# Performance work log

Measured on AMD Instinct MI355X. Metric: run time of the kernel, lower is better.

## Reference

```python
import jax, jax.numpy as jnp
import numpy as np

B = 8192          # batch
LATENT = 32       # latent_dim
H = 64            # hidden_size
SEQ_LEN = 180
NUM_CLASSES = 6
IN = 2            # GRU input size (zeros) / output features


def setup_inputs() -> dict:
    key = jax.random.key(0)
    ks = jax.random.split(key, 12)
    s_fc = 1.0 / np.sqrt(LATENT + H)
    s_rnn = 1.0 / np.sqrt(H)
    return {
        "z": jax.random.normal(ks[0], (B, LATENT), dtype=jnp.float32),
        "labels": jax.random.randint(ks[1], (B,), 0, NUM_CLASSES),
        "embed_w": jax.random.normal(ks[2], (NUM_CLASSES, H), dtype=jnp.float32),
        "fc_w": jax.random.uniform(ks[3], (H, LATENT + H), jnp.float32, -s_fc, s_fc),
        "fc_b": jax.random.uniform(ks[4], (H,), jnp.float32, -s_fc, s_fc),
        "w_ih": jax.random.uniform(ks[5], (3 * H, IN), jnp.float32, -s_rnn, s_rnn),
        "w_hh": jax.random.uniform(ks[6], (3 * H, H), jnp.float32, -s_rnn, s_rnn),
        "b_ih": jax.random.uniform(ks[7], (3 * H,), jnp.float32, -s_rnn, s_rnn),
        "b_hh": jax.random.uniform(ks[8], (3 * H,), jnp.float32, -s_rnn, s_rnn),
        "out_w": jax.random.uniform(ks[9], (IN, H), jnp.float32, -s_rnn, s_rnn),
        "out_b": jax.random.uniform(ks[10], (IN,), jnp.float32, -s_rnn, s_rnn),
    }


def reference(z, labels, embed_w, fc_w, fc_b, w_ih, w_hh, b_ih, b_hh, out_w, out_b):
    # h0 = tanh(fc([z, embed(labels)]))  -> [B, H]
    cond = embed_w[labels]
    h0 = jnp.tanh(jnp.concatenate([z, cond], axis=1) @ fc_w.T + fc_b)

    # GRU input is all zeros, so the input-side gates are constant per step:
    # gi = x_t @ w_ih.T + b_ih = b_ih  (kept faithful to torch GRU math)
    i_r, i_z, i_n = jnp.split(b_ih, 3)

    def step(h, _):
        gh = h @ w_hh.T + b_hh                      # [B, 3H]
        h_r, h_z, h_n = jnp.split(gh, 3, axis=-1)
        r = jax.nn.sigmoid(i_r + h_r)
        zg = jax.nn.sigmoid(i_z + h_z)
        n = jnp.tanh(i_n + r * h_n)
        h_new = (1.0 - zg) * n + zg * h
        return h_new, h_new

    _, hs = jax.lax.scan(step, h0, None, length=SEQ_LEN)  # [S, B, H]
    # out linear: [B, S, 2]
    return jnp.einsum("sbh,oh->bso", hs, out_w) + out_b
```

## Files before the change

kernel.cpp:

```cpp
#include <hip/hip_runtime.h>

#define NBATCH 8192
#define HDIM   64
#define SEQ    180
#define MT     16
#define NC     2
#define SB     72
#define XSP    100

typedef __bf16 bf16x8 __attribute__((ext_vector_type(8)));
typedef __bf16 bf16x4 __attribute__((ext_vector_type(4)));
typedef float  f32x4  __attribute__((ext_vector_type(4)));

#define L2E 1.44269504088896340736f

__device__ __forceinline__ float tanh_f(float x) {
    float e = __builtin_amdgcn_exp2f((2.0f * L2E) * x);
    return 1.0f - 2.0f * __builtin_amdgcn_rcpf(1.0f + e);
}

#define MFMA __builtin_amdgcn_mfma_f32_16x16x32_bf16

__device__ __forceinline__ f32x4 gru_epi(f32x4 aR, f32x4 aZ, f32x4 aN,
        f32x4 cR4, f32x4 cZ4, f32x4 bn4, f32x4 cN4, f32x4 one4,
        f32x4 hprev, __bf16* Nh, int wboff) {
    f32x4 tR = aR * (-L2E) + cR4;
    f32x4 tZ = aZ * (-L2E) + cZ4;
    f32x4 eR, eZ;
#pragma unroll
    for (int r = 0; r < 4; ++r) {
        eR[r] = __builtin_amdgcn_exp2f(tR[r]);
        eZ[r] = __builtin_amdgcn_exp2f(tZ[r]);
    }
    eR = eR + one4;
    eZ = eZ + one4;
    f32x4 rg, zg;
#pragma unroll
    for (int r = 0; r < 4; ++r) {
        rg[r] = __builtin_amdgcn_rcpf(eR[r]);
        zg[r] = __builtin_amdgcn_rcpf(eZ[r]);
    }
    f32x4 mm = aN + bn4;
    f32x4 tN = (rg * mm) * (2.0f * L2E) + cN4;
    f32x4 eN;
#pragma unroll
    for (int r = 0; r < 4; ++r) eN[r] = __builtin_amdgcn_exp2f(tN[r]);
    eN = eN + one4;
    f32x4 dd;
#pragma unroll
    for (int r = 0; r < 4; ++r) dd[r] = __builtin_amdgcn_rcpf(eN[r]);
    f32x4 ng = dd * (-2.0f) + one4;
    f32x4 hn = zg * (hprev - ng) + ng;
    bf16x4 hp;
#pragma unroll
    for (int r = 0; r < 4; ++r) hp[r] = (__bf16)hn[r];
    *(bf16x4*)(Nh + wboff) = hp;
    return hn;
}

__global__ __launch_bounds__(256) void gru_all(
        const float* __restrict__ z, const int* __restrict__ labels,
        const float* __restrict__ embed_w, const float* __restrict__ fc_w,
        const float* __restrict__ fc_b, const float* __restrict__ w_hh,
        const float* __restrict__ b_ih, const float* __restrict__ b_hh,
        const float* __restrict__ out_w, const float* __restrict__ out_b,
        float* __restrict__ out) {
    __shared__ __align__(16) __bf16 hbuf[NC][2][MT * SB];
    __shared__ __align__(16) float  xs[NC * MT * XSP];

    const int t = threadIdx.x;
    const int w = t >> 6;
    const int l = t & 63;
    const int q = l >> 4;
    const int n16 = l & 15;
    const int jg = 16 * w + n16;
    const int jb = 16 * w + 4 * q;
    const int bbase = blockIdx.x * (NC * MT);

    for (int c = t; c < NC * MT * 24; c += 256) {
        int m = c / 24, kk = (c % 24) * 4;
        f32x4 v;
        if (kk < 32) v = *(const f32x4*)(z + (size_t)(bbase + m) * 32 + kk);
        else         v = *(const f32x4*)(embed_w + labels[bbase + m] * 64 + (kk - 32));
        *(f32x4*)(xs + m * XSP + kk) = v;
    }

    bf16x8 whi[3][2];
#pragma unroll
    for (int g = 0; g < 3; ++g) {
        const float* pr = w_hh + (g * 64 + jg) * HDIM;
#pragma unroll
        for (int ks = 0; ks < 2; ++ks) {
            const float* p = pr + ks * 32 + q * 8;
            f32x4 va = *(const f32x4*)(p);
            f32x4 vb = *(const f32x4*)(p + 4);
#pragma unroll
            for (int j2 = 0; j2 < 4; ++j2) {
                whi[g][ks][j2]     = (__bf16)va[j2];
                whi[g][ks][4 + j2] = (__bf16)vb[j2];
            }
        }
    }

    bf16x8 obhi[2];
#pragma unroll
    for (int ks = 0; ks < 2; ++ks) {
        f32x4 va = {0.f, 0.f, 0.f, 0.f}, vb = {0.f, 0.f, 0.f, 0.f};
        if (n16 < 2) {
            va = *(const f32x4*)(out_w + n16 * 64 + ks * 32 + q * 8);
            vb = *(const f32x4*)(out_w + n16 * 64 + ks * 32 + q * 8 + 4);
        }
#pragma unroll
        for (int j2 = 0; j2 < 4; ++j2) {
            obhi[ks][j2]     = (__bf16)va[j2];
            obhi[ks][4 + j2] = (__bf16)vb[j2];
        }
    }
    const f32x4 obias = (q == 0) ? f32x4{out_b[0], out_b[1], 0.f, 0.f}
                                 : f32x4{0.f, 0.f, 0.f, 0.f};
    const f32x4 kZ = {0.f, 0.f, 0.f, 0.f};
    const f32x4 one4 = {1.f, 1.f, 1.f, 1.f};

    const bool ostorer = (q == 0) && ((n16 >> 2) == w);

    const f32x4 bihR = *(const f32x4*)(b_ih + jb);
    const f32x4 bhhR = *(const f32x4*)(b_hh + jb);
    const f32x4 bihZ = *(const f32x4*)(b_ih + 64 + jb);
    const f32x4 bhhZ = *(const f32x4*)(b_hh + 64 + jb);
    const f32x4 cR4 = (bihR + bhhR) * (-L2E);
    const f32x4 cZ4 = (bihZ + bhhZ) * (-L2E);
    const f32x4 bn4 = *(const f32x4*)(b_hh + 128 + jb);
    const f32x4 cN4 = (*(const f32x4*)(b_ih + 128 + jb)) * (2.0f * L2E);

    const int rdoff = n16 * SB + q * 8;
    const int wboff = n16 * SB + jb;
    float* opbA = out + (size_t)(bbase + n16) * (SEQ * 2);
    float* opbB = out + (size_t)(bbase + MT + n16) * (SEQ * 2);

    __syncthreads();

    f32x4 hpA, hpB;
    {
        f32x4 aA = *(const f32x4*)(fc_b + jb);
        f32x4 aB = aA;
        for (int kc = 0; kc < 24; ++kc) {
            f32x4 xvA = *(const f32x4*)(xs + n16 * XSP + kc * 4);
            f32x4 xvB = *(const f32x4*)(xs + (MT + n16) * XSP + kc * 4);
#pragma unroll
            for (int r = 0; r < 4; ++r) {
                f32x4 wv = *(const f32x4*)(fc_w + (size_t)(jb + r) * 96 + kc * 4);
                aA[r] += wv[0] * xvA[0] + wv[1] * xvA[1] + wv[2] * xvA[2] + wv[3] * xvA[3];
                aB[r] += wv[0] * xvB[0] + wv[1] * xvB[1] + wv[2] * xvB[2] + wv[3] * xvB[3];
            }
        }
        bf16x4 ha, hb;
#pragma unroll
        for (int r = 0; r < 4; ++r) {
            hpA[r] = tanh_f(aA[r]); ha[r] = (__bf16)hpA[r];
            hpB[r] = tanh_f(aB[r]); hb[r] = (__bf16)hpB[r];
        }
        *(bf16x4*)(hbuf[0][0] + wboff) = ha;
        *(bf16x4*)(hbuf[1][0] + wboff) = hb;
    }
    __syncthreads();

    for (int u = 0; u < SEQ / 2; ++u) {
#pragma unroll
        for (int s = 0; s < 2; ++s) {
            const __bf16* HA = hbuf[0][s];
            __bf16*       NA = hbuf[0][s ^ 1];
            const __bf16* HB = hbuf[1][s];
            __bf16*      NhB = hbuf[1][s ^ 1];

            bf16x8 a0 = *(const bf16x8*)(HA + rdoff);
            bf16x8 a1 = *(const bf16x8*)(HA + rdoff + 32);
            bf16x8 c0 = *(const bf16x8*)(HB + rdoff);
            bf16x8 c1 = *(const bf16x8*)(HB + rdoff + 32);

            f32x4 ArA = MFMA(whi[0][0], a0, kZ, 0, 0, 0);
            f32x4 AzA = MFMA(whi[1][0], a0, kZ, 0, 0, 0);
            f32x4 AnA = MFMA(whi[2][0], a0, kZ, 0, 0, 0);
            f32x4 ArB = MFMA(whi[0][0], c0, kZ, 0, 0, 0);
            f32x4 AzB = MFMA(whi[1][0], c0, kZ, 0, 0, 0);
            f32x4 AnB = MFMA(whi[2][0], c0, kZ, 0, 0, 0);
            ArA = MFMA(whi[0][1], a1, ArA, 0, 0, 0);
            AzA = MFMA(whi[1][1], a1, AzA, 0, 0, 0);
            AnA = MFMA(whi[2][1], a1, AnA, 0, 0, 0);
            ArB = MFMA(whi[0][1], c1, ArB, 0, 0, 0);
            AzB = MFMA(whi[1][1], c1, AzB, 0, 0, 0);
            AnB = MFMA(whi[2][1], c1, AnB, 0, 0, 0);

            {
                f32x4 oA = obias;
                oA = MFMA(obhi[0], a0, oA, 0, 0, 0);
                oA = MFMA(obhi[1], a1, oA, 0, 0, 0);
                f32x4 oB = obias;
                oB = MFMA(obhi[0], c0, oB, 0, 0, 0);
                oB = MFMA(obhi[1], c1, oB, 0, 0, 0);
                if ((u | s) != 0 && ostorer) {
                    *(float2*)(opbA + (4 * u + 2 * s - 2)) = make_float2(oA[0], oA[1]);
                    *(float2*)(opbB + (4 * u + 2 * s - 2)) = make_float2(oB[0], oB[1]);
                }
            }

            hpA = gru_epi(ArA, AzA, AnA, cR4, cZ4, bn4, cN4, one4, hpA, NA,  wboff);
            hpB = gru_epi(ArB, AzB, AnB, cR4, cZ4, bn4, cN4, one4, hpB, NhB, wboff);

            __syncthreads();
        }
    }

    {
        bf16x8 a0 = *(const bf16x8*)(hbuf[0][0] + rdoff);
        bf16x8 a1 = *(const bf16x8*)(hbuf[0][0] + rdoff + 32);
        bf16x8 c0 = *(const bf16x8*)(hbuf[1][0] + rdoff);
        bf16x8 c1 = *(const bf16x8*)(hbuf[1][0] + rdoff + 32);
        f32x4 oA = obias;
        oA = MFMA(obhi[0], a0, oA, 0, 0, 0);
        oA = MFMA(obhi[1], a1, oA, 0, 0, 0);
        f32x4 oB = obias;
        oB = MFMA(obhi[0], c0, oB, 0, 0, 0);
        oB = MFMA(obhi[1], c1, oB, 0, 0, 0);
        if (ostorer) {
            *(float2*)(opbA + (SEQ - 1) * 2) = make_float2(oA[0], oA[1]);
            *(float2*)(opbB + (SEQ - 1) * 2) = make_float2(oB[0], oB[1]);
        }
    }
}

extern "C" void kernel_launch(void* const* d_in, const int* in_sizes, int n_in,
                              void* d_out, int out_size, void* d_ws, size_t ws_size,
                              hipStream_t stream) {
    (void)in_sizes; (void)n_in; (void)out_size; (void)d_ws; (void)ws_size;
    const float* z       = (const float*)d_in[0];
    const int*   labels  = (const int*)d_in[1];
    const float* embed_w = (const float*)d_in[2];
    const float* fc_w    = (const float*)d_in[3];
    const float* fc_b    = (const float*)d_in[4];
    const float* w_hh    = (const float*)d_in[6];
    const float* b_ih    = (const float*)d_in[7];
    const float* b_hh    = (const float*)d_in[8];
    const float* out_w   = (const float*)d_in[9];
    const float* out_b   = (const float*)d_in[10];
    float* out = (float*)d_out;

    gru_all<<<NBATCH / (NC * MT), 256, 0, stream>>>(z, labels, embed_w, fc_w, fc_b,
                                                    w_hh, b_ih, b_hh, out_w, out_b, out);
}
```

Before: 189.9 us.

## Defer output projection a step, merge GRU epilogue divisions, use LDS-only barrier

The output projection for the previous step's hidden state is now computed with registers kept from the prior iteration, issued before the current gate MFMAs. This takes it off the critical path between the LDS read and the gate math. The GRU update is rewritten so the z-gate sigmoid and the tanh combine into a single reciprocal, cutting the transcendental count. The batch A/B epilogues are interleaved and the inner loop is unrolled by 4. __syncthreads is replaced by an inline s_waitcnt lgkmcnt(0)+s_barrier, which risks subtle ordering issues and adds register pressure from the saved operands.

```diff
diff --git a/kernel.cpp b/kernel.cpp
--- a/kernel.cpp
+++ b/kernel.cpp
@@ -1,6 +1,6 @@
 #include <hip/hip_runtime.h>
 
-#define NBATCH 8192
+#define NB     8192
 #define HDIM   64
 #define SEQ    180
 #define MT     16
@@ -21,42 +21,7 @@
 
 #define MFMA __builtin_amdgcn_mfma_f32_16x16x32_bf16
 
-__device__ __forceinline__ f32x4 gru_epi(f32x4 aR, f32x4 aZ, f32x4 aN,
-        f32x4 cR4, f32x4 cZ4, f32x4 bn4, f32x4 cN4, f32x4 one4,
-        f32x4 hprev, __bf16* Nh, int wboff) {
-    f32x4 tR = aR * (-L2E) + cR4;
-    f32x4 tZ = aZ * (-L2E) + cZ4;
-    f32x4 eR, eZ;
-#pragma unroll
-    for (int r = 0; r < 4; ++r) {
-        eR[r] = __builtin_amdgcn_exp2f(tR[r]);
-        eZ[r] = __builtin_amdgcn_exp2f(tZ[r]);
-    }
-    eR = eR + one4;
-    eZ = eZ + one4;
-    f32x4 rg, zg;
-#pragma unroll
-    for (int r = 0; r < 4; ++r) {
-        rg[r] = __builtin_amdgcn_rcpf(eR[r]);
-        zg[r] = __builtin_amdgcn_rcpf(eZ[r]);
-    }
-    f32x4 mm = aN + bn4;
-    f32x4 tN = (rg * mm) * (2.0f * L2E) + cN4;
-    f32x4 eN;
-#pragma unroll
-    for (int r = 0; r < 4; ++r) eN[r] = __builtin_amdgcn_exp2f(tN[r]);
-    eN = eN + one4;
-    f32x4 dd;
-#pragma unroll
-    for (int r = 0; r < 4; ++r) dd[r] = __builtin_amdgcn_rcpf(eN[r]);
-    f32x4 ng = dd * (-2.0f) + one4;
-    f32x4 hn = zg * (hprev - ng) + ng;
-    bf16x4 hp;
-#pragma unroll
-    for (int r = 0; r < 4; ++r) hp[r] = (__bf16)hn[r];
-    *(bf16x4*)(Nh + wboff) = hp;
-    return hn;
-}
+#define BAR_LDS() asm volatile("s_waitcnt lgkmcnt(0)\n\ts_barrier" ::: "memory")
 
 __global__ __launch_bounds__(256) void gru_all(
         const float* __restrict__ z, const int* __restrict__ labels,
@@ -164,66 +129,131 @@
     }
     __syncthreads();
 
-    for (int u = 0; u < SEQ / 2; ++u) {
-#pragma unroll
-        for (int s = 0; s < 2; ++s) {
-            const __bf16* HA = hbuf[0][s];
-            __bf16*       NA = hbuf[0][s ^ 1];
-            const __bf16* HB = hbuf[1][s];
-            __bf16*      NhB = hbuf[1][s ^ 1];
+    bf16x8 paA0 = {}, paA1 = {}, paB0 = {}, paB1 = {};
+
+    for (int u = 0; u < SEQ / 4; ++u) {
+#pragma unroll
+        for (int s = 0; s < 4; ++s) {
+            const int p = s & 1;
+            const __bf16* HA = hbuf[0][p];
+            __bf16*       NA = hbuf[0][1 - p];
+            const __bf16* HB = hbuf[1][p];
+            __bf16*      NhB = hbuf[1][1 - p];
 
             bf16x8 a0 = *(const bf16x8*)(HA + rdoff);
             bf16x8 a1 = *(const bf16x8*)(HA + rdoff + 32);
             bf16x8 c0 = *(const bf16x8*)(HB + rdoff);
             bf16x8 c1 = *(const bf16x8*)(HB + rdoff + 32);
 
-            f32x4 ArA = MFMA(whi[0][0], a0, kZ, 0, 0, 0);
-            f32x4 AzA = MFMA(whi[1][0], a0, kZ, 0, 0, 0);
-            f32x4 AnA = MFMA(whi[2][0], a0, kZ, 0, 0, 0);
-            f32x4 ArB = MFMA(whi[0][0], c0, kZ, 0, 0, 0);
-            f32x4 AzB = MFMA(whi[1][0], c0, kZ, 0, 0, 0);
-            f32x4 AnB = MFMA(whi[2][0], c0, kZ, 0, 0, 0);
-            ArA = MFMA(whi[0][1], a1, ArA, 0, 0, 0);
-            AzA = MFMA(whi[1][1], a1, AzA, 0, 0, 0);
-            AnA = MFMA(whi[2][1], a1, AnA, 0, 0, 0);
-            ArB = MFMA(whi[0][1], c1, ArB, 0, 0, 0);
-            AzB = MFMA(whi[1][1], c1, AzB, 0, 0, 0);
-            AnB = MFMA(whi[2][1], c1, AnB, 0, 0, 0);
-
             {
-                f32x4 oA = obias;
-                oA = MFMA(obhi[0], a0, oA, 0, 0, 0);
-                oA = MFMA(obhi[1], a1, oA, 0, 0, 0);
-                f32x4 oB = obias;
-                oB = MFMA(obhi[0], c0, oB, 0, 0, 0);
-                oB = MFMA(obhi[1], c1, oB, 0, 0, 0);
-                if ((u | s) != 0 && ostorer) {
-                    *(float2*)(opbA + (4 * u + 2 * s - 2)) = make_float2(oA[0], oA[1]);
-                    *(float2*)(opbB + (4 * u + 2 * s - 2)) = make_float2(oB[0], oB[1]);
+                f32x4 oA = obias, oB = obias;
+                oA = MFMA(obhi[0], paA0, oA, 0, 0, 0);
+                oB = MFMA(obhi[0], paB0, oB, 0, 0, 0);
+                oA = MFMA(obhi[1], paA1, oA, 0, 0, 0);
+                oB = MFMA(obhi[1], paB1, oB, 0, 0, 0);
+                if ((u > 0 || s >= 2) && ostorer) {
+                    *(float2*)(opbA + (8 * u + 2 * s - 4)) = make_float2(oA[0], oA[1]);
+                    *(float2*)(opbB + (8 * u + 2 * s - 4)) = make_float2(oB[0], oB[1]);
                 }
             }
 
-            hpA = gru_epi(ArA, AzA, AnA, cR4, cZ4, bn4, cN4, one4, hpA, NA,  wboff);
-            hpB = gru_epi(ArB, AzB, AnB, cR4, cZ4, bn4, cN4, one4, hpB, NhB, wboff);
-
-            __syncthreads();
+            f32x4 aRA = MFMA(whi[0][0], a0, kZ, 0, 0, 0);
+            f32x4 aRB = MFMA(whi[0][0], c0, kZ, 0, 0, 0);
+            f32x4 aZA = MFMA(whi[1][0], a0, kZ, 0, 0, 0);
+            f32x4 aZB = MFMA(whi[1][0], c0, kZ, 0, 0, 0);
+            f32x4 aNA = MFMA(whi[2][0], a0, kZ, 0, 0, 0);
+            f32x4 aNB = MFMA(whi[2][0], c0, kZ, 0, 0, 0);
+            aRA = MFMA(whi[0][1], a1, aRA, 0, 0, 0);
+            aRB = MFMA(whi[0][1], c1, aRB, 0, 0, 0);
+            aZA = MFMA(whi[1][1], a1, aZA, 0, 0, 0);
+            aZB = MFMA(whi[1][1], c1, aZB, 0, 0, 0);
+            aNA = MFMA(whi[2][1], a1, aNA, 0, 0, 0);
+            aNB = MFMA(whi[2][1], c1, aNB, 0, 0, 0);
+
+            f32x4 tRA = aRA * (-L2E) + cR4;
+            f32x4 tRB = aRB * (-L2E) + cR4;
+            f32x4 tZA = aZA * (-L2E) + cZ4;
+            f32x4 tZB = aZB * (-L2E) + cZ4;
+            f32x4 eRA, eRB, eZA, eZB;
+#pragma unroll
+            for (int r = 0; r < 4; ++r) {
+                eRA[r] = __builtin_amdgcn_exp2f(tRA[r]);
+                eRB[r] = __builtin_amdgcn_exp2f(tRB[r]);
+                eZA[r] = __builtin_amdgcn_exp2f(tZA[r]);
+                eZB[r] = __builtin_amdgcn_exp2f(tZB[r]);
+            }
+            f32x4 AA = eRA + one4;
+            f32x4 AB = eRB + one4;
+            f32x4 rgA, rgB;
+#pragma unroll
+            for (int r = 0; r < 4; ++r) {
+                rgA[r] = __builtin_amdgcn_rcpf(AA[r]);
+                rgB[r] = __builtin_amdgcn_rcpf(AB[r]);
+            }
+            f32x4 mmA = aNA + bn4;
+            f32x4 mmB = aNB + bn4;
+            f32x4 tNA = (rgA * mmA) * (2.0f * L2E) + cN4;
+            f32x4 tNB = (rgB * mmB) * (2.0f * L2E) + cN4;
+            f32x4 eNA, eNB;
+#pragma unroll
+            for (int r = 0; r < 4; ++r) {
+                eNA[r] = __builtin_amdgcn_exp2f(tNA[r]);
+                eNB[r] = __builtin_amdgcn_exp2f(tNB[r]);
+            }
+            f32x4 wzA = eZA + one4,  wzB = eZB + one4;
+            f32x4 pzA = eZA + hpA,   pzB = eZB + hpB;
+            f32x4 qzA = hpA - eZA,   qzB = hpB - eZB;
+            f32x4 NsA = eNA * pzA + qzA;
+            f32x4 NsB = eNB * pzB + qzB;
+            f32x4 DsA = eNA * wzA + wzA;
+            f32x4 DsB = eNB * wzB + wzB;
+            f32x4 rDA, rDB;
+#pragma unroll
+            for (int r = 0; r < 4; ++r) {
+                rDA[r] = __builtin_amdgcn_rcpf(DsA[r]);
+                rDB[r] = __builtin_amdgcn_rcpf(DsB[r]);
+            }
+            f32x4 hnA = NsA * rDA;
+            f32x4 hnB = NsB * rDB;
+            hpA = hnA; hpB = hnB;
+            bf16x4 ha, hb;
+#pragma unroll
+            for (int r = 0; r < 4; ++r) {
+                ha[r] = (__bf16)hnA[r];
+                hb[r] = (__bf16)hnB[r];
+            }
+            *(bf16x4*)(NA  + wboff) = ha;
+            *(bf16x4*)(NhB + wboff) = hb;
+
+            paA0 = a0; paA1 = a1; paB0 = c0; paB1 = c1;
+
+            BAR_LDS();
         }
     }
 
     {
+        f32x4 oA = obias, oB = obias;
+        oA = MFMA(obhi[0], paA0, oA, 0, 0, 0);
+        oB = MFMA(obhi[0], paB0, oB, 0, 0, 0);
+        oA = MFMA(obhi[1], paA1, oA, 0, 0, 0);
+        oB = MFMA(obhi[1], paB1, oB, 0, 0, 0);
+        if (ostorer) {
+            *(float2*)(opbA + (SEQ - 2) * 2) = make_float2(oA[0], oA[1]);
+            *(float2*)(opbB + (SEQ - 2) * 2) = make_float2(oB[0], oB[1]);
+        }
+
         bf16x8 a0 = *(const bf16x8*)(hbuf[0][0] + rdoff);
         bf16x8 a1 = *(const bf16x8*)(hbuf[0][0] + rdoff + 32);
         bf16x8 c0 = *(const bf16x8*)(hbuf[1][0] + rdoff);
         bf16x8 c1 = *(const bf16x8*)(hbuf[1][0] + rdoff + 32);
-        f32x4 oA = obias;
-        oA = MFMA(obhi[0], a0, oA, 0, 0, 0);
-        oA = MFMA(obhi[1], a1, oA, 0, 0, 0);
-        f32x4 oB = obias;
-        oB = MFMA(obhi[0], c0, oB, 0, 0, 0);
-        oB = MFMA(obhi[1], c1, oB, 0, 0, 0);
+        f32x4 o2A = obias, o2B = obias;
+        o2A = MFMA(obhi[0], a0, o2A, 0, 0, 0);
+        o2B = MFMA(obhi[0], c0, o2B, 0, 0, 0);
+        o2A = MFMA(obhi[1], a1, o2A, 0, 0, 0);
+        o2B = MFMA(obhi[1], c1, o2B, 0, 0, 0);
         if (ostorer) {
-            *(float2*)(opbA + (SEQ - 1) * 2) = make_float2(oA[0], oA[1]);
-            *(float2*)(opbB + (SEQ - 1) * 2) = make_float2(oB[0], oB[1]);
+            *(float2*)(opbA + (SEQ - 1) * 2) = make_float2(o2A[0], o2A[1]);
+            *(float2*)(opbB + (SEQ - 1) * 2) = make_float2(o2B[0], o2B[1]);
         }
     }
 }
@@ -244,6 +274,6 @@
     const float* out_b   = (const float*)d_in[10];
     float* out = (float*)d_out;
 
-    gru_all<<<NBATCH / (NC * MT), 256, 0, stream>>>(z, labels, embed_w, fc_w, fc_b,
-                                                    w_hh, b_ih, b_hh, out_w, out_b, out);
+    gru_all<<<NB / (NC * MT), 256, 0, stream>>>(z, labels, embed_w, fc_w, fc_b,
+                                                w_hh, b_ih, b_hh, out_w, out_b, out);
 }
```

New measurement: 173.6 us. 1.09x faster.

## Stagger two batch chains so MFMA of one overlaps epilogue of other

Applied to the files above, without the earlier changes.

Restructures the recurrent loop so the two independent batch halves are offset by a half step: each phase issues the matrix products for one chain while running the gate epilogue for the other, with a barrier per half-step. The epilogue algebra is also reworked to merge the z-gate sigmoid and the tanh into a single reciprocal of a combined denominator, cutting transcendental reciprocals. The barrier is replaced by an inline-asm lgkmcnt wait plus s_barrier. This doubles the number of barriers per step, and the merged-division form may change rounding slightly.

```diff
diff --git a/kernel.cpp b/kernel.cpp
--- a/kernel.cpp
+++ b/kernel.cpp
@@ -1,6 +1,6 @@
 #include <hip/hip_runtime.h>
 
-#define NBATCH 8192
+#define NB     8192
 #define HDIM   64
 #define SEQ    180
 #define MT     16
@@ -21,36 +21,37 @@
 
 #define MFMA __builtin_amdgcn_mfma_f32_16x16x32_bf16
 
-__device__ __forceinline__ f32x4 gru_epi(f32x4 aR, f32x4 aZ, f32x4 aN,
+#define BAR_LDS() asm volatile("s_waitcnt lgkmcnt(0)\n\ts_barrier" ::: "memory")
+
+__device__ __forceinline__ f32x4 epi_write(f32x4 aR, f32x4 aZ, f32x4 aN,
         f32x4 cR4, f32x4 cZ4, f32x4 bn4, f32x4 cN4, f32x4 one4,
         f32x4 hprev, __bf16* Nh, int wboff) {
-    f32x4 tR = aR * (-L2E) + cR4;
-    f32x4 tZ = aZ * (-L2E) + cZ4;
+    f32x4 tRv = aR * (-L2E) + cR4;
+    f32x4 tZv = aZ * (-L2E) + cZ4;
     f32x4 eR, eZ;
 #pragma unroll
     for (int r = 0; r < 4; ++r) {
-        eR[r] = __builtin_amdgcn_exp2f(tR[r]);
-        eZ[r] = __builtin_amdgcn_exp2f(tZ[r]);
-    }
-    eR = eR + one4;
-    eZ = eZ + one4;
-    f32x4 rg, zg;
-#pragma unroll
-    for (int r = 0; r < 4; ++r) {
-        rg[r] = __builtin_amdgcn_rcpf(eR[r]);
-        zg[r] = __builtin_amdgcn_rcpf(eZ[r]);
-    }
+        eR[r] = __builtin_amdgcn_exp2f(tRv[r]);
+        eZ[r] = __builtin_amdgcn_exp2f(tZv[r]);
+    }
+    f32x4 A = eR + one4;
+    f32x4 rg;
+#pragma unroll
+    for (int r = 0; r < 4; ++r) rg[r] = __builtin_amdgcn_rcpf(A[r]);
     f32x4 mm = aN + bn4;
     f32x4 tN = (rg * mm) * (2.0f * L2E) + cN4;
     f32x4 eN;
 #pragma unroll
     for (int r = 0; r < 4; ++r) eN[r] = __builtin_amdgcn_exp2f(tN[r]);
-    eN = eN + one4;
-    f32x4 dd;
-#pragma unroll
-    for (int r = 0; r < 4; ++r) dd[r] = __builtin_amdgcn_rcpf(eN[r]);
-    f32x4 ng = dd * (-2.0f) + one4;
-    f32x4 hn = zg * (hprev - ng) + ng;
+    f32x4 wz = eZ + one4;
+    f32x4 pz = eZ + hprev;
+    f32x4 qz = hprev - eZ;
+    f32x4 Ns = eN * pz + qz;
+    f32x4 Ds = eN * wz + wz;
+    f32x4 rD;
+#pragma unroll
+    for (int r = 0; r < 4; ++r) rD[r] = __builtin_amdgcn_rcpf(Ds[r]);
+    f32x4 hn = Ns * rD;
     bf16x4 hp;
 #pragma unroll
     for (int r = 0; r < 4; ++r) hp[r] = (__bf16)hn[r];
@@ -164,67 +165,105 @@
     }
     __syncthreads();
 
-    for (int u = 0; u < SEQ / 2; ++u) {
-#pragma unroll
-        for (int s = 0; s < 2; ++s) {
-            const __bf16* HA = hbuf[0][s];
-            __bf16*       NA = hbuf[0][s ^ 1];
-            const __bf16* HB = hbuf[1][s];
-            __bf16*      NhB = hbuf[1][s ^ 1];
-
-            bf16x8 a0 = *(const bf16x8*)(HA + rdoff);
-            bf16x8 a1 = *(const bf16x8*)(HA + rdoff + 32);
-            bf16x8 c0 = *(const bf16x8*)(HB + rdoff);
-            bf16x8 c1 = *(const bf16x8*)(HB + rdoff + 32);
-
-            f32x4 ArA = MFMA(whi[0][0], a0, kZ, 0, 0, 0);
-            f32x4 AzA = MFMA(whi[1][0], a0, kZ, 0, 0, 0);
-            f32x4 AnA = MFMA(whi[2][0], a0, kZ, 0, 0, 0);
-            f32x4 ArB = MFMA(whi[0][0], c0, kZ, 0, 0, 0);
-            f32x4 AzB = MFMA(whi[1][0], c0, kZ, 0, 0, 0);
-            f32x4 AnB = MFMA(whi[2][0], c0, kZ, 0, 0, 0);
-            ArA = MFMA(whi[0][1], a1, ArA, 0, 0, 0);
-            AzA = MFMA(whi[1][1], a1, AzA, 0, 0, 0);
-            AnA = MFMA(whi[2][1], a1, AnA, 0, 0, 0);
-            ArB = MFMA(whi[0][1], c1, ArB, 0, 0, 0);
-            AzB = MFMA(whi[1][1], c1, AzB, 0, 0, 0);
-            AnB = MFMA(whi[2][1], c1, AnB, 0, 0, 0);
+    bf16x8 paA0 = {}, paA1 = {};
+    bf16x8 paB0, paB1;
+    f32x4 aRA, aZA, aNA, aRB, aZB, aNB;
+    {
+        const __bf16* HB = hbuf[1][0];
+        paB0 = *(const bf16x8*)(HB + rdoff);
+        paB1 = *(const bf16x8*)(HB + rdoff + 32);
+        aRB = MFMA(whi[0][0], paB0, kZ, 0, 0, 0);
+        aZB = MFMA(whi[1][0], paB0, kZ, 0, 0, 0);
+        aNB = MFMA(whi[2][0], paB0, kZ, 0, 0, 0);
+        aRB = MFMA(whi[0][1], paB1, aRB, 0, 0, 0);
+        aZB = MFMA(whi[1][1], paB1, aZB, 0, 0, 0);
+        aNB = MFMA(whi[2][1], paB1, aNB, 0, 0, 0);
+    }
+
+    for (int tt = 0; tt < SEQ / 2; ++tt) {
+#pragma unroll
+        for (int par = 0; par < 2; ++par) {
+            const int ts = 2 * tt + par;
 
             {
-                f32x4 oA = obias;
-                oA = MFMA(obhi[0], a0, oA, 0, 0, 0);
-                oA = MFMA(obhi[1], a1, oA, 0, 0, 0);
-                f32x4 oB = obias;
-                oB = MFMA(obhi[0], c0, oB, 0, 0, 0);
-                oB = MFMA(obhi[1], c1, oB, 0, 0, 0);
-                if ((u | s) != 0 && ostorer) {
-                    *(float2*)(opbA + (4 * u + 2 * s - 2)) = make_float2(oA[0], oA[1]);
-                    *(float2*)(opbB + (4 * u + 2 * s - 2)) = make_float2(oB[0], oB[1]);
+                const __bf16* HA = hbuf[0][par];
+                __bf16*      nbp = hbuf[1][par ^ 1];
+                bf16x8 a0 = *(const bf16x8*)(HA + rdoff);
+                bf16x8 a1 = *(const bf16x8*)(HA + rdoff + 32);
+
+                {
+                    f32x4 o = obias;
+                    o = MFMA(obhi[0], paA0, o, 0, 0, 0);
+                    o = MFMA(obhi[1], paA1, o, 0, 0, 0);
+                    if (ts >= 2 && ostorer)
+                        *(float2*)(opbA + (ts - 2) * 2) = make_float2(o[0], o[1]);
                 }
-            }
-
-            hpA = gru_epi(ArA, AzA, AnA, cR4, cZ4, bn4, cN4, one4, hpA, NA,  wboff);
-            hpB = gru_epi(ArB, AzB, AnB, cR4, cZ4, bn4, cN4, one4, hpB, NhB, wboff);
-
-            __syncthreads();
+
+                f32x4 nR = MFMA(whi[0][0], a0, kZ, 0, 0, 0);
+                f32x4 nZ = MFMA(whi[1][0], a0, kZ, 0, 0, 0);
+                f32x4 nN = MFMA(whi[2][0], a0, kZ, 0, 0, 0);
+                nR = MFMA(whi[0][1], a1, nR, 0, 0, 0);
+                nZ = MFMA(whi[1][1], a1, nZ, 0, 0, 0);
+                nN = MFMA(whi[2][1], a1, nN, 0, 0, 0);
+
+                hpB = epi_write(aRB, aZB, aNB, cR4, cZ4, bn4, cN4, one4,
+                                hpB, nbp, wboff);
+
+                aRA = nR; aZA = nZ; aNA = nN;
+                paA0 = a0; paA1 = a1;
+                BAR_LDS();
+            }
+
+            {
+                const __bf16* HB = hbuf[1][par ^ 1];
+                __bf16*      nap = hbuf[0][par ^ 1];
+                bf16x8 c0 = *(const bf16x8*)(HB + rdoff);
+                bf16x8 c1 = *(const bf16x8*)(HB + rdoff + 32);
+
+                {
+                    f32x4 o = obias;
+                    o = MFMA(obhi[0], paB0, o, 0, 0, 0);
+                    o = MFMA(obhi[1], paB1, o, 0, 0, 0);
+                    if (ts >= 1 && ostorer)
+                        *(float2*)(opbB + (ts - 1) * 2) = make_float2(o[0], o[1]);
+                }
+
+                f32x4 nR = MFMA(whi[0][0], c0, kZ, 0, 0, 0);
+                f32x4 nZ = MFMA(whi[1][0], c0, kZ, 0, 0, 0);
+                f32x4 nN = MFMA(whi[2][0], c0, kZ, 0, 0, 0);
+                nR = MFMA(whi[0][1], c1, nR, 0, 0, 0);
+                nZ = MFMA(whi[1][1], c1, nZ, 0, 0, 0);
+                nN = MFMA(whi[2][1], c1, nN, 0, 0, 0);
+
+                hpA = epi_write(aRA, aZA, aNA, cR4, cZ4, bn4, cN4, one4,
+                                hpA, nap, wboff);
+
+                aRB = nR; aZB = nZ; aNB = nN;
+                paB0 = c0; paB1 = c1;
+                BAR_LDS();
+            }
         }
     }
 
     {
-        bf16x8 a0 = *(const bf16x8*)(hbuf[0][0] + rdoff);
-        bf16x8 a1 = *(const bf16x8*)(hbuf[0][0] + rdoff + 32);
-        bf16x8 c0 = *(const bf16x8*)(hbuf[1][0] + rdoff);
-        bf16x8 c1 = *(const bf16x8*)(hbuf[1][0] + rdoff + 32);
         f32x4 oA = obias;
-        oA = MFMA(obhi[0], a0, oA, 0, 0, 0);
-        oA = MFMA(obhi[1], a1, oA, 0, 0, 0);
+        oA = MFMA(obhi[0], paA0, oA, 0, 0, 0);
+        oA = MFMA(obhi[1], paA1, oA, 0, 0, 0);
         f32x4 oB = obias;
-        oB = MFMA(obhi[0], c0, oB, 0, 0, 0);
-        oB = MFMA(obhi[1], c1, oB, 0, 0, 0);
+        oB = MFMA(obhi[0], paB0, oB, 0, 0, 0);
+        oB = MFMA(obhi[1], paB1, oB, 0, 0, 0);
         if (ostorer) {
-            *(float2*)(opbA + (SEQ - 1) * 2) = make_float2(oA[0], oA[1]);
+            *(float2*)(opbA + (SEQ - 2) * 2) = make_float2(oA[0], oA[1]);
             *(float2*)(opbB + (SEQ - 1) * 2) = make_float2(oB[0], oB[1]);
         }
+        const __bf16* HA = hbuf[0][0];
+        bf16x8 a0 = *(const bf16x8*)(HA + rdoff);
+        bf16x8 a1 = *(const bf16x8*)(HA + rdoff + 32);
+        f32x4 o2 = obias;
+        o2 = MFMA(obhi[0], a0, o2, 0, 0, 0);
+        o2 = MFMA(obhi[1], a1, o2, 0, 0, 0);
+        if (ostorer)
+            *(float2*)(opbA + (SEQ - 1) * 2) = make_float2(o2[0], o2[1]);
     }
 }
 
@@ -244,6 +283,6 @@
     const float* out_b   = (const float*)d_in[10];
     float* out = (float*)d_out;
 
-    gru_all<<<NBATCH / (NC * MT), 256, 0, stream>>>(z, labels, embed_w, fc_w, fc_b,
-                                                    w_hh, b_ih, b_hh, out_w, out_b, out);
-}
+    gru_all<<<NB / (NC * MT), 256, 0, stream>>>(z, labels, embed_w, fc_w, fc_b,
+                                                w_hh, b_ih, b_hh, out_w, out_b, out);
+}
```

Result: no change. 193.4 us (+1.9%).
